# Performance work log

Measured on AMD Instinct MI355X. Metric: run time of the kernel, lower is better.

The kernel has to match this reference:

```python
import jax, jax.numpy as jnp
import numpy as np


def log_g(x):
    # log of g(x) = x+0.5 if x>=0 else sigmoid(x)
    return jnp.where(x >= 0, jnp.log(jax.nn.relu(x) + 0.5), -jax.nn.softplus(-x))


def setup_inputs() -> dict:
    key = jax.random.key(0)
    B, T, D, H = 8, 4096, 1024, 1024
    ks = jax.random.split(key, 7)
    s = 1.0 / np.sqrt(D)
    return {
        "x": jax.random.normal(ks[0], (B, T, D), dtype=jnp.float32),
        "h0": jnp.zeros((B, 1, H), dtype=jnp.float32),
        "W_f": jax.random.uniform(ks[1], (H, D), jnp.float32, -s, s),
        "b_f": jax.random.uniform(ks[2], (H,), jnp.float32, -s, s),
        "W_i": jax.random.uniform(ks[3], (H, D), jnp.float32, -s, s),
        "b_i": jax.random.uniform(ks[4], (H,), jnp.float32, -s, s),
        "W_h": jax.random.uniform(ks[5], (H, D), jnp.float32, -s, s),
        "b_h": jax.random.uniform(ks[6], (H,), jnp.float32, -s, s),
    }


def reference(x, h0, W_f, b_f, W_i, b_i, W_h, b_h):
    # gate pre-activations: [B, T, H]
    zf = jnp.einsum("btd,hd->bth", x, W_f) + b_f
    zi = jnp.einsum("btd,hd->bth", x, W_i) + b_i
    zh = jnp.einsum("btd,hd->bth", x, W_h) + b_h
    diff = jax.nn.softplus(-zf) - jax.nn.softplus(-zi)
    log_f = -jax.nn.softplus(diff)        # log f'_t
    log_i = -jax.nn.softplus(-diff)       # log i'_t
    log_values = jnp.concatenate([log_g(h0), log_i + log_g(zh)], axis=1)  # [B, T+1, H]
    # parallel scan in log space
    a_star = jnp.pad(jnp.cumsum(log_f, axis=1), ((0, 0), (1, 0), (0, 0)))  # [B, T+1, H]
    log_h = a_star + jax.lax.cumlogsumexp(log_values - a_star, axis=1)
    return jnp.exp(log_h)[:, 1:]  # [B, T, H]
```

## Files before the change

kernel.cpp:

```cpp
#include <hip/hip_runtime.h>
#include <hip/hip_bf16.h>
#include <stdint.h>
#include <stddef.h>

#define B_ 8
#define T_ 4096
#define D_ 1024
#define H_ 1024
#define M_ (B_*T_)
#define K_ 1024
#define CHUNK 32
#define NCHUNK 128
#define NWGF ((M_/128)*(H_/128))

typedef __attribute__((ext_vector_type(8))) __bf16 bf16v8;
typedef __attribute__((ext_vector_type(4))) float f32x4;
typedef __attribute__((ext_vector_type(8))) unsigned short u16x8;

#define QA  0
#define QBF 16384
#define QBI 32768
#define QBH 49152
#define SLOT 65536
#define LDS_BYTES 131072

#define FENCE() asm volatile("" ::: "memory")
#define SBAR()  __builtin_amdgcn_s_barrier()
#define STG(p, d) __builtin_amdgcn_global_load_lds(                        \
    (const __attribute__((address_space(1))) void*)(p),                    \
    (__attribute__((address_space(3))) void*)(d), 16, 0, 0)

__device__ __forceinline__ unsigned short f2bf(float f) {
  union { float f; unsigned u; } x; x.f = f;
  return (unsigned short)((x.u + 0x7fffu + ((x.u >> 16) & 1u)) >> 16);
}

__global__ __launch_bounds__(256) void cvt_x(const float* __restrict__ src,
                                             unsigned short* __restrict__ dst) {
  int i = blockIdx.x * 256 + threadIdx.x;
  const float4* s = (const float4*)src;
  float4 a = s[i*2], b = s[i*2+1];
  u16x8 o;
  o[0]=f2bf(a.x); o[1]=f2bf(a.y); o[2]=f2bf(a.z); o[3]=f2bf(a.w);
  o[4]=f2bf(b.x); o[5]=f2bf(b.y); o[6]=f2bf(b.z); o[7]=f2bf(b.w);
  *(u16x8*)(dst + (size_t)i*8) = o;
}

__global__ __launch_bounds__(256) void cvt_w(const float* __restrict__ w0,
                                             const float* __restrict__ w1,
                                             const float* __restrict__ w2,
                                             unsigned short* __restrict__ dst) {
  int i = blockIdx.x * 256 + threadIdx.x;
  int seg = i >> 17;
  int off = i & 131071;
  const float* src = (seg == 0) ? w0 : (seg == 1) ? w1 : w2;
  const float4* s = (const float4*)src;
  float4 a = s[off*2], b = s[off*2+1];
  u16x8 o;
  o[0]=f2bf(a.x); o[1]=f2bf(a.y); o[2]=f2bf(a.z); o[3]=f2bf(a.w);
  o[4]=f2bf(b.x); o[5]=f2bf(b.y); o[6]=f2bf(b.z); o[7]=f2bf(b.w);
  *(u16x8*)(dst + (size_t)i*8) = o;
}

__device__ __forceinline__ void rdA8(const char* rbase, int wm, int lr, int cbL,
                                     bf16v8 af[4][2]) {
  #pragma unroll
  for (int i = 0; i < 4; ++i)
    #pragma unroll
    for (int kk = 0; kk < 2; ++kk) {
      int rr = wm*64 + i*16 + lr;
      int cb = kk*64 + cbL;
      af[i][kk] = *(const bf16v8*)(rbase + rr*128 + (cb ^ ((rr & 7) << 4)));
    }
}

__device__ __forceinline__ void rdB4(const char* rbase, int wn, int lr, int cbL,
                                     bf16v8 b[2][2]) {
  #pragma unroll
  for (int j = 0; j < 2; ++j)
    #pragma unroll
    for (int kk = 0; kk < 2; ++kk) {
      int rr = wn*32 + j*16 + lr;
      int cb = kk*64 + cbL;
      b[j][kk] = *(const bf16v8*)(rbase + rr*128 + (cb ^ ((rr & 7) << 4)));
    }
}

__device__ __forceinline__ void mm16(f32x4 acc[4][2], bf16v8 af[4][2],
                                     bf16v8 b[2][2]) {
  __builtin_amdgcn_s_setprio(1);
  #pragma unroll
  for (int i = 0; i < 4; ++i)
    #pragma unroll
    for (int j = 0; j < 2; ++j)
      #pragma unroll
      for (int kk = 0; kk < 2; ++kk)
        acc[i][j] = __builtin_amdgcn_mfma_f32_16x16x32_bf16(af[i][kk], b[j][kk], acc[i][j], 0, 0, 0);
  __builtin_amdgcn_s_setprio(0);
}

__device__ __forceinline__ void gate_eval(float vzf, float vzi, float vzh,
                                          float& f, float& v) {
  float spf = fmaxf(-vzf, 0.f) + __logf(1.f + __expf(-fabsf(vzf)));
  float spi = fmaxf(-vzi, 0.f) + __logf(1.f + __expf(-fabsf(vzi)));
  float d   = spf - spi;
  float l1  = __logf(1.f + __expf(-fabsf(d)));
  f = __expf(-(fmaxf(d, 0.f) + l1));
  float iv = __expf(-(fmaxf(-d, 0.f) + l1));
  float gv = (vzh >= 0.f) ? (vzh + 0.5f) : 1.f/(1.f + __expf(-vzh));
  v = iv * gv;
}

#define STEP_FULL(RD, SOFF, KB)                                              \
  {                                                                          \
    const char* rd = smem + (RD)*SLOT;                                       \
    rdA8(rd + QA,  wm, lr, cbL, af);                                         \
    rdB4(rd + QBF, wn, lr, cbL, bF);                                         \
    STG(pA0 + (KB), dA0 + (SOFF)); STG(pA1 + (KB), dA1 + (SOFF));            \
    STG(pF0 + (KB), dF0 + (SOFF)); STG(pF1 + (KB), dF1 + (SOFF));            \
    FENCE();                                                                 \
    mm16(accF, af, bF);                                                      \
    asm volatile("s_waitcnt vmcnt(6)" ::: "memory"); SBAR(); FENCE();        \
    rdB4(rd + QBI, wn, lr, cbL, bI);                                         \
    STG(pI0 + (KB), dI0 + (SOFF)); STG(pI1 + (KB), dI1 + (SOFF));            \
    FENCE();                                                                 \
    mm16(accI, af, bI);                                                      \
    asm volatile("s_waitcnt vmcnt(6)" ::: "memory"); SBAR(); FENCE();        \
    rdB4(rd + QBH, wn, lr, cbL, bH);                                         \
    STG(pH0 + (KB), dH0 + (SOFF)); STG(pH1 + (KB), dH1 + (SOFF));            \
    FENCE();                                                                 \
    mm16(accH, af, bH);                                                      \
    asm volatile("s_waitcnt vmcnt(4)" ::: "memory"); SBAR(); FENCE();        \
  }

__global__ __launch_bounds__(512, 2) void gemm_fused(
    const unsigned short* __restrict__ Abf,
    const unsigned short* __restrict__ Wc,
    const float* __restrict__ bf_, const float* __restrict__ bi_,
    const float* __restrict__ bh_,
    uint32_t* __restrict__ fv)
{
  extern __shared__ char smem[];
  int tid = threadIdx.x;
  int bid = blockIdx.x;
  int swz = (bid & 7) * (NWGF/8) + (bid >> 3);
  int tn = swz & 7, tm = swz >> 3;
  int m0 = tm*128, n0 = tn*128;
  int lane = tid & 63, wid = tid >> 6;
  int wm = wid >> 2, wn = wid & 3;
  int lr = lane & 15, lhi = lane >> 4;
  int cbL = lhi * 16;

  const unsigned short* Ag  = Abf + (size_t)m0 * K_;
  const unsigned short* BFg = Wc + (size_t)n0 * K_;
  const unsigned short* BIg = Wc + (size_t)(H_ + n0) * K_;
  const unsigned short* BHg = Wc + (size_t)(2*H_ + n0) * K_;

  int o0 = tid*16, o1 = o0 + 8192;
  int r0 = o0 >> 7, c0 = o0 & 127;
  int r1 = o1 >> 7, c1 = o1 & 127;
  size_t lo0 = (size_t)r0*K_ + (size_t)((c0 ^ ((r0 & 7) << 4)) >> 1);
  size_t lo1 = (size_t)r1*K_ + (size_t)((c1 ^ ((r1 & 7) << 4)) >> 1);
  const char* pA0 = (const char*)(Ag  + lo0);
  const char* pA1 = (const char*)(Ag  + lo1);
  const char* pF0 = (const char*)(BFg + lo0);
  const char* pF1 = (const char*)(BFg + lo1);
  const char* pI0 = (const char*)(BIg + lo0);
  const char* pI1 = (const char*)(BIg + lo1);
  const char* pH0 = (const char*)(BHg + lo0);
  const char* pH1 = (const char*)(BHg + lo1);
  char* dA0 = smem + QA  + o0;  char* dA1 = smem + QA  + o1;
  char* dF0 = smem + QBF + o0;  char* dF1 = smem + QBF + o1;
  char* dI0 = smem + QBI + o0;  char* dI1 = smem + QBI + o1;
  char* dH0 = smem + QBH + o0;  char* dH1 = smem + QBH + o1;

  f32x4 accF[4][2] = {}, accI[4][2] = {}, accH[4][2] = {};
  bf16v8 af[4][2], bF[2][2], bI[2][2], bH[2][2];

  STG(pA0, dA0); STG(pA1, dA1);
  STG(pF0, dF0); STG(pF1, dF1);
  STG(pI0, dI0); STG(pI1, dI1);
  STG(pH0, dH0); STG(pH1, dH1);
  pA0 += 128; pA1 += 128; pF0 += 128; pF1 += 128;
  pI0 += 128; pI1 += 128; pH0 += 128; pH1 += 128;
  asm volatile("s_waitcnt vmcnt(4)" ::: "memory");
  SBAR(); FENCE();

  for (int tt = 0; tt < 7; ++tt) {
    STEP_FULL(0, SLOT, 0)
    STEP_FULL(1, 0, 128)
    pA0 += 256; pA1 += 256; pF0 += 256; pF1 += 256;
    pI0 += 256; pI1 += 256; pH0 += 256; pH1 += 256;
  }
  STEP_FULL(0, SLOT, 0)
  {
    const char* rd = smem + SLOT;
    rdA8(rd + QA,  wm, lr, cbL, af);
    rdB4(rd + QBF, wn, lr, cbL, bF);
    FENCE();
    mm16(accF, af, bF);
    asm volatile("s_waitcnt vmcnt(2)" ::: "memory"); SBAR(); FENCE();
    rdB4(rd + QBI, wn, lr, cbL, bI);
    FENCE();
    mm16(accI, af, bI);
    asm volatile("s_waitcnt vmcnt(0)" ::: "memory"); SBAR(); FENCE();
    rdB4(rd + QBH, wn, lr, cbL, bH);
    FENCE();
    mm16(accH, af, bH);
  }

  float bfv[2], biv[2], bhv[2];
  #pragma unroll
  for (int j = 0; j < 2; ++j) {
    int col = n0 + wn*32 + j*16 + lr;
    bfv[j] = bf_[col]; biv[j] = bi_[col]; bhv[j] = bh_[col];
  }
  #pragma unroll
  for (int i = 0; i < 4; ++i)
    #pragma unroll
    for (int j = 0; j < 2; ++j) {
      int col = n0 + wn*32 + j*16 + lr;
      int row0 = m0 + wm*64 + i*16 + lhi*4;
      #pragma unroll
      for (int r = 0; r < 4; ++r) {
        float f, v;
        gate_eval(accF[i][j][r] + bfv[j], accI[i][j][r] + biv[j],
                  accH[i][j][r] + bhv[j], f, v);
        fv[(size_t)(row0 + r)*H_ + col] =
            (uint32_t)f2bf(f) | ((uint32_t)f2bf(v) << 16);
      }
    }
}

__global__ __launch_bounds__(256) void scan_phaseA(
    const uint32_t* __restrict__ fv,
    float* __restrict__ Aw, float* __restrict__ Sw)
{
  int blk = blockIdx.x;
  int c = blk & 127, b = blk >> 7;
  int h4 = threadIdx.x * 4;
  size_t base = ((size_t)b*T_ + (size_t)c*CHUNK)*H_ + h4;
  float Ap[4] = {1.f,1.f,1.f,1.f}, S[4] = {0.f,0.f,0.f,0.f};
  uint4 pk = *(const uint4*)(fv + base);
  for (int t = 0; t < CHUNK; ++t) {
    uint4 nx = pk;
    if (t + 1 < CHUNK) nx = *(const uint4*)(fv + base + (size_t)(t+1)*H_);
    uint32_t w[4] = {pk.x, pk.y, pk.z, pk.w};
    #pragma unroll
    for (int u = 0; u < 4; ++u) {
      union { uint32_t u; float f; } cf, cv;
      cf.u = (w[u] & 0xffffu) << 16;
      cv.u = w[u] & 0xffff0000u;
      S[u] = fmaf(cf.f, S[u], cv.f);
      Ap[u] *= cf.f;
    }
    pk = nx;
  }
  size_t widx = ((size_t)b*NCHUNK + c)*H_ + h4;
  *(float4*)(Aw + widx) = make_float4(Ap[0], Ap[1], Ap[2], Ap[3]);
  *(float4*)(Sw + widx) = make_float4(S[0], S[1], S[2], S[3]);
}

__global__ __launch_bounds__(256) void scan_phaseB(
    const float* __restrict__ Aw, const float* __restrict__ Sw,
    const float* __restrict__ h0, float* __restrict__ Cw)
{
  int i = blockIdx.x*256 + threadIdx.x;
  int b = i >> 8;
  int h4 = (i & 255) * 4;
  float4 x0 = *(const float4*)(h0 + (size_t)b*H_ + h4);
  float run[4];
  const float* px = (const float*)&x0;
  #pragma unroll
  for (int u = 0; u < 4; ++u)
    run[u] = (px[u] >= 0.f) ? (px[u] + 0.5f) : 1.f/(1.f + __expf(-px[u]));
  for (int c = 0; c < NCHUNK; ++c) {
    size_t idx = ((size_t)b*NCHUNK + c)*H_ + h4;
    *(float4*)(Cw + idx) = make_float4(run[0], run[1], run[2], run[3]);
    float4 av = *(const float4*)(Aw + idx);
    float4 sv = *(const float4*)(Sw + idx);
    const float* pa = (const float*)&av;
    const float* ps = (const float*)&sv;
    #pragma unroll
    for (int u = 0; u < 4; ++u) run[u] = fmaf(pa[u], run[u], ps[u]);
  }
}

__global__ __launch_bounds__(256) void scan_phaseC(
    const uint32_t* __restrict__ fv, const float* __restrict__ Cw,
    float* __restrict__ out)
{
  int blk = blockIdx.x;
  int c = blk & 127, b = blk >> 7;
  int h4 = threadIdx.x * 4;
  float4 cw = *(const float4*)(Cw + ((size_t)b*NCHUNK + c)*H_ + h4);
  float hh[4];
  const float* pc = (const float*)&cw;
  #pragma unroll
  for (int u = 0; u < 4; ++u) hh[u] = pc[u];
  size_t base = ((size_t)b*T_ + (size_t)c*CHUNK)*H_ + h4;
  uint4 pk = *(const uint4*)(fv + base);
  for (int t = 0; t < CHUNK; ++t) {
    uint4 nx = pk;
    if (t + 1 < CHUNK) nx = *(const uint4*)(fv + base + (size_t)(t+1)*H_);
    uint32_t w[4] = {pk.x, pk.y, pk.z, pk.w};
    #pragma unroll
    for (int u = 0; u < 4; ++u) {
      union { uint32_t u; float f; } cf, cv;
      cf.u = (w[u] & 0xffffu) << 16;
      cv.u = w[u] & 0xffff0000u;
      hh[u] = fmaf(cf.f, hh[u], cv.f);
    }
    *(float4*)(out + base + (size_t)t*H_) = make_float4(hh[0], hh[1], hh[2], hh[3]);
    pk = nx;
  }
}

extern "C" void kernel_launch(void* const* d_in, const int* in_sizes, int n_in,
                              void* d_out, int out_size, void* d_ws, size_t ws_size,
                              hipStream_t stream) {
  const float* x   = (const float*)d_in[0];
  const float* h0  = (const float*)d_in[1];
  const float* W_f = (const float*)d_in[2];
  const float* b_f = (const float*)d_in[3];
  const float* W_i = (const float*)d_in[4];
  const float* b_i = (const float*)d_in[5];
  const float* W_h = (const float*)d_in[6];
  const float* b_h = (const float*)d_in[7];
  float* out = (float*)d_out;

  char* ws = (char*)d_ws;
  unsigned short* xb = (unsigned short*)ws;
  unsigned short* Wc = (unsigned short*)(ws + (size_t)M_*K_*2);
  uint32_t* fv = (uint32_t*)(ws + (size_t)M_*K_*2 + (size_t)3*H_*K_*2);
  float* Aw = (float*)(fv + (size_t)M_*H_);
  float* Sw = Aw + (size_t)B_*NCHUNK*H_;
  float* Cw = Sw + (size_t)B_*NCHUNK*H_;

  (void)hipFuncSetAttribute((const void*)gemm_fused,
      hipFuncAttributeMaxDynamicSharedMemorySize, LDS_BYTES);

  cvt_x<<<M_*K_/8/256, 256, 0, stream>>>(x, xb);
  cvt_w<<<3*H_*K_/8/256, 256, 0, stream>>>(W_f, W_i, W_h, Wc);

  gemm_fused<<<NWGF, 512, LDS_BYTES, stream>>>(xb, Wc, b_f, b_i, b_h, fv);

  scan_phaseA<<<B_*NCHUNK, 256, 0, stream>>>(fv, Aw, Sw);
  scan_phaseB<<<B_*H_/4/256, 256, 0, stream>>>(Aw, Sw, h0, Cw);
  scan_phaseC<<<B_*NCHUNK, 256, 0, stream>>>(fv, Cw, out);
}
```

Before: 588.5 us.

## Restructure GEMM k-loop pipelining, merge conversion kernels, double scan chunk size

The GEMM main loop now issues one full wait and barrier per K step, then stages the whole next tile at once and runs all three MFMA groups back to back under raised priority. The staggered per-gate waits and barriers are gone. The two bf16 conversion kernels are merged into a single launch. The scan uses 64-step chunks instead of 32, drops manual prefetch in favour of unroll-8 loops, and unrolls the phase B loop. The coarser GEMM synchronisation may expose more global-load latency, and the longer chunks halve the scan's block-level parallelism.

```diff
diff --git a/kernel.cpp b/kernel.cpp
--- a/kernel.cpp
+++ b/kernel.cpp
@@ -9,8 +9,8 @@
 #define H_ 1024
 #define M_ (B_*T_)
 #define K_ 1024
-#define CHUNK 32
-#define NCHUNK 128
+#define CHUNK 64
+#define NCHUNK 64
 #define NWGF ((M_/128)*(H_/128))
 
 typedef __attribute__((ext_vector_type(8))) __bf16 bf16v8;
@@ -35,31 +35,26 @@
   return (unsigned short)((x.u + 0x7fffu + ((x.u >> 16) & 1u)) >> 16);
 }
 
-__global__ __launch_bounds__(256) void cvt_x(const float* __restrict__ src,
-                                             unsigned short* __restrict__ dst) {
+__global__ __launch_bounds__(256) void cvt_all(
+    const float* __restrict__ x,
+    const float* __restrict__ w0, const float* __restrict__ w1,
+    const float* __restrict__ w2,
+    unsigned short* __restrict__ xb, unsigned short* __restrict__ wb) {
   int i = blockIdx.x * 256 + threadIdx.x;
-  const float4* s = (const float4*)src;
-  float4 a = s[i*2], b = s[i*2+1];
-  u16x8 o;
-  o[0]=f2bf(a.x); o[1]=f2bf(a.y); o[2]=f2bf(a.z); o[3]=f2bf(a.w);
-  o[4]=f2bf(b.x); o[5]=f2bf(b.y); o[6]=f2bf(b.z); o[7]=f2bf(b.w);
-  *(u16x8*)(dst + (size_t)i*8) = o;
-}
-
-__global__ __launch_bounds__(256) void cvt_w(const float* __restrict__ w0,
-                                             const float* __restrict__ w1,
-                                             const float* __restrict__ w2,
-                                             unsigned short* __restrict__ dst) {
-  int i = blockIdx.x * 256 + threadIdx.x;
-  int seg = i >> 17;
-  int off = i & 131071;
-  const float* src = (seg == 0) ? w0 : (seg == 1) ? w1 : w2;
+  const int NX = M_*K_/8;
+  const float* src; unsigned short* dst; int off;
+  if (i < NX) { src = x; dst = xb; off = i; }
+  else {
+    int j = i - NX; int seg = j >> 17; off = j & 131071;
+    src = (seg == 0) ? w0 : (seg == 1) ? w1 : w2;
+    dst = wb + (size_t)seg * H_ * K_;
+  }
   const float4* s = (const float4*)src;
   float4 a = s[off*2], b = s[off*2+1];
   u16x8 o;
   o[0]=f2bf(a.x); o[1]=f2bf(a.y); o[2]=f2bf(a.z); o[3]=f2bf(a.w);
   o[4]=f2bf(b.x); o[5]=f2bf(b.y); o[6]=f2bf(b.z); o[7]=f2bf(b.w);
-  *(u16x8*)(dst + (size_t)i*8) = o;
+  *(u16x8*)(dst + (size_t)off*8) = o;
 }
 
 __device__ __forceinline__ void rdA8(const char* rbase, int wm, int lr, int cbL,
@@ -88,7 +83,6 @@
 
 __device__ __forceinline__ void mm16(f32x4 acc[4][2], bf16v8 af[4][2],
                                      bf16v8 b[2][2]) {
-  __builtin_amdgcn_s_setprio(1);
   #pragma unroll
   for (int i = 0; i < 4; ++i)
     #pragma unroll
@@ -96,7 +90,6 @@
       #pragma unroll
       for (int kk = 0; kk < 2; ++kk)
         acc[i][j] = __builtin_amdgcn_mfma_f32_16x16x32_bf16(af[i][kk], b[j][kk], acc[i][j], 0, 0, 0);
-  __builtin_amdgcn_s_setprio(0);
 }
 
 __device__ __forceinline__ void gate_eval(float vzf, float vzi, float vzh,
@@ -111,26 +104,27 @@
   v = iv * gv;
 }
 
-#define STEP_FULL(RD, SOFF, KB)                                              \
+#define KSTEP(RD, SOFF, KB, ST)                                              \
   {                                                                          \
+    asm volatile("s_waitcnt vmcnt(0)" ::: "memory");                         \
+    SBAR(); FENCE();                                                         \
+    if (ST) {                                                                \
+      STG(pA0 + (KB), dA0 + (SOFF)); STG(pA1 + (KB), dA1 + (SOFF));          \
+      STG(pF0 + (KB), dF0 + (SOFF)); STG(pF1 + (KB), dF1 + (SOFF));          \
+      STG(pI0 + (KB), dI0 + (SOFF)); STG(pI1 + (KB), dI1 + (SOFF));          \
+      STG(pH0 + (KB), dH0 + (SOFF)); STG(pH1 + (KB), dH1 + (SOFF));          \
+    }                                                                        \
+    FENCE();                                                                 \
     const char* rd = smem + (RD)*SLOT;                                       \
     rdA8(rd + QA,  wm, lr, cbL, af);                                         \
     rdB4(rd + QBF, wn, lr, cbL, bF);                                         \
-    STG(pA0 + (KB), dA0 + (SOFF)); STG(pA1 + (KB), dA1 + (SOFF));            \
-    STG(pF0 + (KB), dF0 + (SOFF)); STG(pF1 + (KB), dF1 + (SOFF));            \
-    FENCE();                                                                 \
+    rdB4(rd + QBI, wn, lr, cbL, bI);                                         \
+    rdB4(rd + QBH, wn, lr, cbL, bH);                                         \
+    __builtin_amdgcn_s_setprio(1);                                           \
     mm16(accF, af, bF);                                                      \
-    asm volatile("s_waitcnt vmcnt(6)" ::: "memory"); SBAR(); FENCE();        \
-    rdB4(rd + QBI, wn, lr, cbL, bI);                                         \
-    STG(pI0 + (KB), dI0 + (SOFF)); STG(pI1 + (KB), dI1 + (SOFF));            \
-    FENCE();                                                                 \
     mm16(accI, af, bI);                                                      \
-    asm volatile("s_waitcnt vmcnt(6)" ::: "memory"); SBAR(); FENCE();        \
-    rdB4(rd + QBH, wn, lr, cbL, bH);                                         \
-    STG(pH0 + (KB), dH0 + (SOFF)); STG(pH1 + (KB), dH1 + (SOFF));            \
-    FENCE();                                                                 \
     mm16(accH, af, bH);                                                      \
-    asm volatile("s_waitcnt vmcnt(4)" ::: "memory"); SBAR(); FENCE();        \
+    __builtin_amdgcn_s_setprio(0);                                           \
   }
 
 __global__ __launch_bounds__(512, 2) void gemm_fused(
@@ -183,31 +177,15 @@
   STG(pH0, dH0); STG(pH1, dH1);
   pA0 += 128; pA1 += 128; pF0 += 128; pF1 += 128;
   pI0 += 128; pI1 += 128; pH0 += 128; pH1 += 128;
-  asm volatile("s_waitcnt vmcnt(4)" ::: "memory");
-  SBAR(); FENCE();
 
   for (int tt = 0; tt < 7; ++tt) {
-    STEP_FULL(0, SLOT, 0)
-    STEP_FULL(1, 0, 128)
+    KSTEP(0, SLOT, 0, 1)
+    KSTEP(1, 0, 128, 1)
     pA0 += 256; pA1 += 256; pF0 += 256; pF1 += 256;
     pI0 += 256; pI1 += 256; pH0 += 256; pH1 += 256;
   }
-  STEP_FULL(0, SLOT, 0)
-  {
-    const char* rd = smem + SLOT;
-    rdA8(rd + QA,  wm, lr, cbL, af);
-    rdB4(rd + QBF, wn, lr, cbL, bF);
-    FENCE();
-    mm16(accF, af, bF);
-    asm volatile("s_waitcnt vmcnt(2)" ::: "memory"); SBAR(); FENCE();
-    rdB4(rd + QBI, wn, lr, cbL, bI);
-    FENCE();
-    mm16(accI, af, bI);
-    asm volatile("s_waitcnt vmcnt(0)" ::: "memory"); SBAR(); FENCE();
-    rdB4(rd + QBH, wn, lr, cbL, bH);
-    FENCE();
-    mm16(accH, af, bH);
-  }
+  KSTEP(0, SLOT, 0, 1)
+  KSTEP(1, 0, 128, 0)
 
   float bfv[2], biv[2], bhv[2];
   #pragma unroll
@@ -237,14 +215,13 @@
     float* __restrict__ Aw, float* __restrict__ Sw)
 {
   int blk = blockIdx.x;
-  int c = blk & 127, b = blk >> 7;
+  int c = blk & 63, b = blk >> 6;
   int h4 = threadIdx.x * 4;
   size_t base = ((size_t)b*T_ + (size_t)c*CHUNK)*H_ + h4;
   float Ap[4] = {1.f,1.f,1.f,1.f}, S[4] = {0.f,0.f,0.f,0.f};
-  uint4 pk = *(const uint4*)(fv + base);
+  #pragma unroll 8
   for (int t = 0; t < CHUNK; ++t) {
-    uint4 nx = pk;
-    if (t + 1 < CHUNK) nx = *(const uint4*)(fv + base + (size_t)(t+1)*H_);
+    uint4 pk = *(const uint4*)(fv + base + (size_t)t*H_);
     uint32_t w[4] = {pk.x, pk.y, pk.z, pk.w};
     #pragma unroll
     for (int u = 0; u < 4; ++u) {
@@ -254,7 +231,6 @@
       S[u] = fmaf(cf.f, S[u], cv.f);
       Ap[u] *= cf.f;
     }
-    pk = nx;
   }
   size_t widx = ((size_t)b*NCHUNK + c)*H_ + h4;
   *(float4*)(Aw + widx) = make_float4(Ap[0], Ap[1], Ap[2], Ap[3]);
@@ -274,6 +250,7 @@
   #pragma unroll
   for (int u = 0; u < 4; ++u)
     run[u] = (px[u] >= 0.f) ? (px[u] + 0.5f) : 1.f/(1.f + __expf(-px[u]));
+  #pragma unroll 8
   for (int c = 0; c < NCHUNK; ++c) {
     size_t idx = ((size_t)b*NCHUNK + c)*H_ + h4;
     *(float4*)(Cw + idx) = make_float4(run[0], run[1], run[2], run[3]);
@@ -291,7 +268,7 @@
     float* __restrict__ out)
 {
   int blk = blockIdx.x;
-  int c = blk & 127, b = blk >> 7;
+  int c = blk & 63, b = blk >> 6;
   int h4 = threadIdx.x * 4;
   float4 cw = *(const float4*)(Cw + ((size_t)b*NCHUNK + c)*H_ + h4);
   float hh[4];
@@ -299,10 +276,10 @@
   #pragma unroll
   for (int u = 0; u < 4; ++u) hh[u] = pc[u];
   size_t base = ((size_t)b*T_ + (size_t)c*CHUNK)*H_ + h4;
-  uint4 pk = *(const uint4*)(fv + base);
+  #pragma unroll 8
   for (int t = 0; t < CHUNK; ++t) {
-    uint4 nx = pk;
-    if (t + 1 < CHUNK) nx = *(const uint4*)(fv + base + (size_t)(t+1)*H_);
+    size_t idx = base + (size_t)t*H_;
+    uint4 pk = *(const uint4*)(fv + idx);
     uint32_t w[4] = {pk.x, pk.y, pk.z, pk.w};
     #pragma unroll
     for (int u = 0; u < 4; ++u) {
@@ -311,8 +288,7 @@
       cv.u = w[u] & 0xffff0000u;
       hh[u] = fmaf(cf.f, hh[u], cv.f);
     }
-    *(float4*)(out + base + (size_t)t*H_) = make_float4(hh[0], hh[1], hh[2], hh[3]);
-    pk = nx;
+    *(float4*)(out + idx) = make_float4(hh[0], hh[1], hh[2], hh[3]);
   }
 }
 
@@ -340,8 +316,7 @@
   (void)hipFuncSetAttribute((const void*)gemm_fused,
       hipFuncAttributeMaxDynamicSharedMemorySize, LDS_BYTES);
 
-  cvt_x<<<M_*K_/8/256, 256, 0, stream>>>(x, xb);
-  cvt_w<<<3*H_*K_/8/256, 256, 0, stream>>>(W_f, W_i, W_h, Wc);
+  cvt_all<<<(M_*K_/8 + 3*H_*K_/8)/256, 256, 0, stream>>>(x, W_f, W_i, W_h, xb, Wc);
 
   gemm_fused<<<NWGF, 512, LDS_BYTES, stream>>>(xb, Wc, b_f, b_i, b_h, fv);
 
```

After: 582.6 us. No clear change (-1.0%).
